# Kernel tuning notes

Hardware: AMD Instinct MI355X
Metric: run time of the kernel (lower is better)

## Reference

```python
import jax, jax.numpy as jnp
import numpy as np

# ----- module hyperparameters (from init_kwargs) -----
C = 21            # num_classes
H = 512           # image_dims[0]
W = 512           # image_dims[1]
THETA_ALPHA = 3.0 # bilateral spatial std
THETA_BETA = 3.0  # bilateral color std
THETA_GAMMA = 3.0 # spatial-only std
NUM_ITERS = 5
R_BIL = int(2 * THETA_ALPHA)   # bilateral window radius (2 sigma truncation)
R_SP = int(2 * THETA_GAMMA)    # spatial Gaussian radius


def _gauss_1d(radius, sigma):
    x = jnp.arange(-radius, radius + 1, dtype=jnp.float32)
    return jnp.exp(-0.5 * (x / sigma) ** 2)  # unnormalized; norm handled by norm_values


def spatial_filter(vals):
    """Separable truncated Gaussian blur over (H,W). vals: (C,H,W)."""
    k = _gauss_1d(R_SP, THETA_GAMMA)
    K = 2 * R_SP + 1
    x = vals[:, None]  # (C,1,H,W) -> treat channels as batch
    kh = k.reshape(1, 1, K, 1)
    kw = k.reshape(1, 1, 1, K)
    x = jax.lax.conv_general_dilated(x, kh, (1, 1), ((R_SP, R_SP), (0, 0)))
    x = jax.lax.conv_general_dilated(x, kw, (1, 1), ((0, 0), (R_SP, R_SP)))
    return x[:, 0]


def _bilateral_impl(vals, rgb):
    """Truncated-window bilateral Gaussian filter.
    vals: (C,H,W) values to filter; rgb: (3,H,W) guide image.
    weight(i,j) = exp(-0.5*(|p_i-p_j|^2/ta^2 + |I_i-I_j|^2/tb^2)) (symmetric kernel).
    """
    pad = R_BIL
    vp = jnp.pad(vals, ((0, 0), (pad, pad), (pad, pad)))
    rp = jnp.pad(rgb, ((0, 0), (pad, pad), (pad, pad)))
    d = jnp.arange(2 * pad + 1, dtype=jnp.int32)
    offs = jnp.stack(jnp.meshgrid(d, d, indexing='ij'), -1).reshape(-1, 2)  # (K^2,2)
    inv_a2 = 1.0 / (THETA_ALPHA ** 2)
    inv_b2 = 1.0 / (THETA_BETA ** 2)

    def step(acc, off):
        dy, dx = off[0], off[1]
        z = dy * 0
        srgb = jax.lax.dynamic_slice(rp, (z, dy, dx), rgb.shape)
        sval = jax.lax.dynamic_slice(vp, (z, dy, dx), vals.shape)
        dsp = ((dy - pad) ** 2 + (dx - pad) ** 2).astype(jnp.float32)
        dcol = jnp.sum((rgb - srgb) ** 2, axis=0)  # (H,W)
        w = jnp.exp(-0.5 * (dsp * inv_a2 + dcol * inv_b2))
        return acc + sval * w[None], None

    out, _ = jax.lax.scan(step, jnp.zeros_like(vals), offs)
    return out


# Symmetric linear operator in vals -> adjoint = same filter. rgb treated as constant
# (no grad to raw image, matching CRF-RNN training). Keeps backward memory O(1) in steps.
@jax.custom_vjp
def bilateral_filter(vals, rgb):
    return _bilateral_impl(vals, rgb)

def _bf_fwd(vals, rgb):
    return _bilateral_impl(vals, rgb), rgb

def _bf_bwd(rgb, g):
    return _bilateral_impl(g, rgb), jnp.zeros_like(rgb)

bilateral_filter.defvjp(_bf_fwd, _bf_bwd)


def setup_inputs() -> dict:
    key = jax.random.key(0)
    k1, k2, k3, k4 = jax.random.split(key, 4)
    unaries = jax.random.normal(k1, (1, H, W, C), jnp.float32)
    rgb = jax.random.uniform(k2, (1, H, W, 3), jnp.float32) * 255.0
    spatial_ker_weights = jax.random.uniform(k3, (C, C), jnp.float32)
    bilateral_ker_weights = jax.random.truncated_normal(k4, -2.0, 2.0, (C, C), jnp.float32)
    compatibility_matrix = -jnp.eye(C, dtype=jnp.float32)
    return {
        'unaries': unaries,
        'rgb': rgb,
        'spatial_ker_weights': spatial_ker_weights,
        'bilateral_ker_weights': bilateral_ker_weights,
        'compatibility_matrix': compatibility_matrix,
    }


def reference(unaries, rgb, spatial_ker_weights, bilateral_ker_weights, compatibility_matrix):
    u = jnp.transpose(unaries[0], (2, 1, 0))   # (C,W,H) as in tf.transpose perm=[2,1,0]
    im = jnp.transpose(rgb[0], (2, 1, 0))      # (3,W,H)
    c, h, w = u.shape
    ones = jnp.ones_like(u)
    sp_norm = spatial_filter(ones)
    bl_norm = bilateral_filter(ones, im)
    q = u
    for _ in range(NUM_ITERS):
        p = jax.nn.softmax(q, axis=0)
        sp = spatial_filter(p) / sp_norm
        bl = bilateral_filter(p, im) / bl_norm
        msg = spatial_ker_weights @ sp.reshape(c, -1) + bilateral_ker_weights @ bl.reshape(c, -1)
        pairwise = (compatibility_matrix @ msg).reshape(c, h, w)
        q = u - pairwise
    return jnp.transpose(q[None], (0, 2, 3, 1))  # (1,h,w,c)
```

## Files before the change

kernel.cpp:

```cpp
#include <hip/hip_runtime.h>
#include <cstddef>

#define HW   512
#define NPIX (HW*HW)
#define NP   (NPIX + 64)
#define NC   21

typedef unsigned int u32;
typedef __fp16 h2 __attribute__((ext_vector_type(2)));

__device__ __forceinline__ float fexp2(float x) { return __builtin_amdgcn_exp2f(x); }
__device__ __forceinline__ h2 as_h2(u32 x) { union { u32 u; h2 h; } v; v.u = x; return v.h; }
__device__ __forceinline__ u32 as_u32(h2 x) { union { h2 h; u32 u; } v; v.h = x; return v.u; }
__device__ __forceinline__ u32 pkrtz(float a, float b) { return as_u32(__builtin_amdgcn_cvt_pkrtz(a, b)); }

__device__ __forceinline__ float dot7(const u32* w, const u32* a, float s) {
    #pragma unroll
    for (int t = 0; t < 7; ++t)
        s = __builtin_amdgcn_fdot2(as_h2(w[t]), as_h2(a[t]), s, false);
    return s;
}

#define KB_EXP (-0.08014972449f)
#define LOG2E  (1.4426950408889634f)

#define KSP_INIT {0.13533528f, 0.24935221f, 0.41111229f, 0.60653066f, 0.80073740f, \
                  0.94595947f, 1.00000000f, 0.94595947f, 0.80073740f, 0.60653066f, \
                  0.41111229f, 0.24935221f, 0.13533528f}

__global__ void k_setup(const float* __restrict__ unaries, const float* __restrict__ rgb,
                        float* __restrict__ u, float* q, float* __restrict__ rgbT,
                        _Float16* u16) {
    int p = blockIdx.x * 256 + threadIdx.x;
    int a = p >> 9, b = p & 511;
    int src = b * 512 + a;
    #pragma unroll
    for (int c = 0; c < NC; ++c) {
        float v = unaries[src * NC + c];
        u[c * NP + p] = v;
        if (q)   q[c * NP + p] = v;
        if (u16) u16[(size_t)c * NPIX + p] = (_Float16)v;
    }
    #pragma unroll
    for (int ch = 0; ch < 3; ++ch) rgbT[ch * NP + p] = rgb[src * 3 + ch];
}

__global__ void k_prep(const float* __restrict__ Wsp, const float* __restrict__ Wbl,
                       const float* __restrict__ Cm,
                       float* __restrict__ invS, float* __restrict__ M1, float* __restrict__ M2) {
    int t = threadIdx.x;
    const float KSP[13] = KSP_INIT;
    {
        float s = 0.f;
        #pragma unroll
        for (int d = 0; d < 13; ++d) {
            int i = t + d - 6;
            if ((unsigned)i < 512u) s += KSP[d];
        }
        invS[t] = 1.0f / s;
    }
    if (t < NC * NC) {
        int c = t / NC, j = t % NC;
        float s1 = 0.f, s2 = 0.f;
        for (int k = 0; k < NC; ++k) {
            float cm = Cm[c * NC + k];
            s1 += cm * Wsp[k * NC + j];
            s2 += cm * Wbl[k * NC + j];
        }
        M1[t] = -s1;
        M2[t] = -s2;
    }
}

__global__ void k_weights(const float* __restrict__ rgbT, u32* __restrict__ wbuf,
                          float* __restrict__ inorm) {
    int a  = blockIdx.x;
    int b0 = threadIdx.x << 2;
    float cr[3][4];
    #pragma unroll
    for (int ch = 0; ch < 3; ++ch) {
        float4 f = *reinterpret_cast<const float4*>(rgbT + ch * NP + a * HW + b0);
        cr[ch][0] = f.x; cr[ch][1] = f.y; cr[ch][2] = f.z; cr[ch][3] = f.w;
    }
    float nsum[4] = {0.f, 0.f, 0.f, 0.f};
    #pragma unroll 1
    for (int dyi = 0; dyi < 13; ++dyi) {
        int ar = a + dyi - 6;
        if ((unsigned)ar >= 512u) continue;
        float nr[3][20];
        #pragma unroll
        for (int ch = 0; ch < 3; ++ch)
            #pragma unroll
            for (int tq = 0; tq < 5; ++tq) {
                float4 f = *reinterpret_cast<const float4*>(rgbT + ch * NP + ar * HW + b0 - 8 + 4 * tq);
                nr[ch][4*tq+0] = f.x; nr[ch][4*tq+1] = f.y; nr[ch][4*tq+2] = f.z; nr[ch][4*tq+3] = f.w;
            }
        float spk = KB_EXP * (float)((dyi - 6) * (dyi - 6));
        u32 arr[28];
        #pragma unroll
        for (int j = 0; j < 4; ++j) {
            float w[13];
            #pragma unroll
            for (int dx = 0; dx < 13; ++dx) {
                int ic = j + dx + 2;
                float d0 = cr[0][j] - nr[0][ic];
                float d1 = cr[1][j] - nr[1][ic];
                float d2 = cr[2][j] - nr[2][ic];
                float dcol = d0*d0 + d1*d1 + d2*d2;
                float arg = KB_EXP * dcol + (spk + KB_EXP * (float)((dx-6)*(dx-6)));
                bool ok = (unsigned)(b0 + j + dx - 6) < 512u;
                w[dx] = ok ? fexp2(arg) : 0.f;
                nsum[j] += w[dx];
            }
            #pragma unroll
            for (int t = 0; t < 6; ++t) arr[j*7+t] = pkrtz(w[2*t], w[2*t+1]);
            arr[j*7+6] = pkrtz(w[12], 0.f);
        }
        uint4* dst = reinterpret_cast<uint4*>(wbuf) + ((size_t)(a * 13 + dyi) * 896 + threadIdx.x * 7);
        #pragma unroll
        for (int k = 0; k < 7; ++k)
            dst[k] = make_uint4(arr[4*k], arr[4*k+1], arr[4*k+2], arr[4*k+3]);
    }
    float4 r;
    r.x = 1.0f / nsum[0]; r.y = 1.0f / nsum[1];
    r.z = 1.0f / nsum[2]; r.w = 1.0f / nsum[3];
    *reinterpret_cast<float4*>(inorm + a * HW + b0) = r;
}

__global__ __launch_bounds__(128, 3)
void k_filters(const _Float16* __restrict__ ph, const u32* __restrict__ wbuf,
               const float* __restrict__ invS,
               _Float16* __restrict__ P, _Float16* __restrict__ SP) {
    int bid = blockIdx.x;
    int xj = bid & 7;
    int g  = bid >> 3;
    int rl = g / 3;
    int y  = g - rl * 3;
    int a  = xj * 64 + rl;
    int cbase = y * 7;
    int tid = threadIdx.x;
    int b0  = tid << 2;

    const float KSP[13] = KSP_INIT;
    u32 kp[4][7];
    #pragma unroll
    for (int j = 0; j < 4; ++j) {
        float wj[13];
        #pragma unroll
        for (int dx = 0; dx < 13; ++dx) {
            bool ok = (unsigned)(b0 + j + dx - 6) < 512u;
            wj[dx] = ok ? KSP[dx] : 0.f;
        }
        #pragma unroll
        for (int t = 0; t < 6; ++t) kp[j][t] = pkrtz(wj[2*t], wj[2*t+1]);
        kp[j][6] = pkrtz(wj[12], 0.f);
    }

    float acc[7][4], spa[7][4];
    #pragma unroll
    for (int ci = 0; ci < 7; ++ci)
        #pragma unroll
        for (int j = 0; j < 4; ++j) { acc[ci][j] = 0.f; spa[ci][j] = 0.f; }

    #pragma unroll 1
    for (int dyi = 0; dyi < 13; ++dyi) {
        int ar = a + dyi - 6;
        if ((unsigned)ar >= 512u) continue;
        float kdy = fexp2(KB_EXP * (float)((dyi - 6) * (dyi - 6)));
        const uint4* wp = reinterpret_cast<const uint4*>(wbuf) + ((size_t)(a * 13 + dyi) * 896 + tid * 7);
        u32 arr[28];
        #pragma unroll
        for (int k = 0; k < 7; ++k) {
            uint4 wv = wp[k];
            arr[4*k] = wv.x; arr[4*k+1] = wv.y; arr[4*k+2] = wv.z; arr[4*k+3] = wv.w;
        }
        #pragma unroll
        for (int ci = 0; ci < 7; ++ci) {
            const uint2* pw = reinterpret_cast<const uint2*>(ph + (size_t)(cbase + ci) * NPIX + ar * HW + b0 - 8);
            uint2 L0 = pw[0], L1 = pw[1], L2 = pw[2], L3 = pw[3], L4 = pw[4];
            u32 W0[10] = {L0.x, L0.y, L1.x, L1.y, L2.x, L2.y, L3.x, L3.y, L4.x, L4.y};
            u32 W1[9];
            #pragma unroll
            for (int k = 1; k < 9; ++k) W1[k] = (W0[k] >> 16) | (W0[k+1] << 16);
            acc[ci][0] = dot7(arr + 0,  W0 + 1, acc[ci][0]);
            acc[ci][1] = dot7(arr + 7,  W1 + 1, acc[ci][1]);
            acc[ci][2] = dot7(arr + 14, W0 + 2, acc[ci][2]);
            acc[ci][3] = dot7(arr + 21, W1 + 2, acc[ci][3]);
            spa[ci][0] = fmaf(kdy, dot7(kp[0], W0 + 1, 0.f), spa[ci][0]);
            spa[ci][1] = fmaf(kdy, dot7(kp[1], W1 + 1, 0.f), spa[ci][1]);
            spa[ci][2] = fmaf(kdy, dot7(kp[2], W0 + 2, 0.f), spa[ci][2]);
            spa[ci][3] = fmaf(kdy, dot7(kp[3], W1 + 2, 0.f), spa[ci][3]);
        }
    }
    float isa = invS[a];
    float4 iv = *reinterpret_cast<const float4*>(invS + b0);
    #pragma unroll
    for (int ci = 0; ci < 7; ++ci) {
        uint2 st;
        st.x = pkrtz(acc[ci][0], acc[ci][1]);
        st.y = pkrtz(acc[ci][2], acc[ci][3]);
        *reinterpret_cast<uint2*>(P + (size_t)(cbase + ci) * NPIX + a * HW + b0) = st;
        uint2 ss;
        ss.x = pkrtz(spa[ci][0] * isa * iv.x, spa[ci][1] * isa * iv.y);
        ss.y = pkrtz(spa[ci][2] * isa * iv.z, spa[ci][3] * isa * iv.w);
        *reinterpret_cast<uint2*>(SP + (size_t)(cbase + ci) * NPIX + a * HW + b0) = ss;
    }
}

__global__ void k_combine2(const float* __restrict__ u, const _Float16* __restrict__ u16,
                           const _Float16* __restrict__ sp, const _Float16* __restrict__ P,
                           const float* __restrict__ inorm,
                           const float* __restrict__ M1, const float* __restrict__ M2,
                           _Float16* __restrict__ phout, float* __restrict__ out, int last) {
    __shared__ float m1[NC * NC], m2[NC * NC];
    int t = threadIdx.x;
    for (int i = t; i < NC * NC; i += 256) { m1[i] = M1[i]; m2[i] = M2[i]; }
    __syncthreads();
    int px = blockIdx.x * 256 + t;
    float rn = inorm[px];
    float msg[NC];
    #pragma unroll
    for (int c = 0; c < NC; ++c) msg[c] = 0.f;
    #pragma unroll 3
    for (int k = 0; k < NC; ++k) {
        float s = (float)sp[(size_t)k * NPIX + px];
        float b = (float)P[(size_t)k * NPIX + px] * rn;
        #pragma unroll
        for (int c = 0; c < NC; ++c) msg[c] += m1[c * NC + k] * s + m2[c * NC + k] * b;
    }
    if (last) {
        #pragma unroll
        for (int c = 0; c < NC; ++c)
            out[(size_t)px * NC + c] = u[c * NP + px] + msg[c];
    } else {
        float qv[NC];
        #pragma unroll
        for (int c = 0; c < NC; ++c) qv[c] = (float)u16[(size_t)c * NPIX + px] + msg[c];
        float m = -1e30f;
        #pragma unroll
        for (int c = 0; c < NC; ++c) m = fmaxf(m, qv[c]);
        float s = 0.f;
        #pragma unroll
        for (int c = 0; c < NC; ++c) { qv[c] = fexp2((qv[c] - m) * LOG2E); s += qv[c]; }
        float r = 1.0f / s;
        #pragma unroll
        for (int c = 0; c < NC; ++c) phout[(size_t)c * NPIX + px] = (_Float16)(qv[c] * r);
    }
}

__global__ void k_softmax(const float* __restrict__ q, _Float16* __restrict__ ph) {
    int i4 = (blockIdx.x * 256 + threadIdx.x) << 2;
    float v[NC][4];
    float m[4] = {-1e30f, -1e30f, -1e30f, -1e30f};
    #pragma unroll
    for (int c = 0; c < NC; ++c) {
        float4 f = *reinterpret_cast<const float4*>(q + c * NP + i4);
        v[c][0] = f.x; v[c][1] = f.y; v[c][2] = f.z; v[c][3] = f.w;
        #pragma unroll
        for (int j = 0; j < 4; ++j) m[j] = fmaxf(m[j], v[c][j]);
    }
    float s[4] = {0.f, 0.f, 0.f, 0.f};
    #pragma unroll
    for (int c = 0; c < NC; ++c)
        #pragma unroll
        for (int j = 0; j < 4; ++j) { v[c][j] = fexp2((v[c][j] - m[j]) * LOG2E); s[j] += v[c][j]; }
    float r[4];
    #pragma unroll
    for (int j = 0; j < 4; ++j) r[j] = 1.0f / s[j];
    #pragma unroll
    for (int c = 0; c < NC; ++c) {
        uint2 st;
        st.x = pkrtz(v[c][0] * r[0], v[c][1] * r[1]);
        st.y = pkrtz(v[c][2] * r[2], v[c][3] * r[3]);
        *reinterpret_cast<uint2*>(ph + (size_t)c * NPIX + i4) = st;
    }
}

__global__ void k_blnorm_part(const float* __restrict__ rgbT, float* __restrict__ nq) {
    int bid = blockIdx.x;
    int z = bid >> 9, a = bid & 511;
    int b0 = threadIdx.x << 2;
    float cr[3][4];
    #pragma unroll
    for (int ch = 0; ch < 3; ++ch) {
        float4 f = *reinterpret_cast<const float4*>(rgbT + ch * NP + a * HW + b0);
        cr[ch][0] = f.x; cr[ch][1] = f.y; cr[ch][2] = f.z; cr[ch][3] = f.w;
    }
    float sum[4] = {0.f, 0.f, 0.f, 0.f};
    const int dylos[4] = {-6, -3, 1, 4};
    const int dyhis[4] = {-4,  0, 3, 6};
    int dylo = dylos[z], dyhi = dyhis[z];
    #pragma unroll 1
    for (int dy = dylo; dy <= dyhi; ++dy) {
        int ar = a + dy;
        if ((unsigned)ar >= 512u) continue;
        int rowoff = ar * HW + b0 - 8;
        float nr[3][20];
        #pragma unroll
        for (int ch = 0; ch < 3; ++ch)
            #pragma unroll
            for (int tq = 0; tq < 5; ++tq) {
                float4 f = *reinterpret_cast<const float4*>(rgbT + ch * NP + rowoff + 4 * tq);
                nr[ch][4*tq+0] = f.x; nr[ch][4*tq+1] = f.y; nr[ch][4*tq+2] = f.z; nr[ch][4*tq+3] = f.w;
            }
        float spk = KB_EXP * (float)(dy * dy);
        #pragma unroll
        for (int j = 0; j < 4; ++j) {
            #pragma unroll
            for (int dx = 0; dx < 13; ++dx) {
                int ic = j + dx + 2;
                float d0 = cr[0][j] - nr[0][ic];
                float d1 = cr[1][j] - nr[1][ic];
                float d2 = cr[2][j] - nr[2][ic];
                float dcol = d0*d0 + d1*d1 + d2*d2;
                float arg = KB_EXP * dcol + (spk + KB_EXP * (float)((dx-6)*(dx-6)));
                bool ok = (unsigned)(b0 + j + dx - 6) < 512u;
                sum[j] += ok ? fexp2(arg) : 0.f;
            }
        }
    }
    float4 r; r.x = sum[0]; r.y = sum[1]; r.z = sum[2]; r.w = sum[3];
    *reinterpret_cast<float4*>(nq + (size_t)z * NP + a * HW + b0) = r;
}

__global__ void k_invnorm(const float* __restrict__ nq, float* __restrict__ inorm) {
    int i = blockIdx.x * 256 + threadIdx.x;
    inorm[i] = 1.0f / (nq[i] + nq[NP + i] + nq[2 * (size_t)NP + i] + nq[3 * (size_t)NP + i]);
}

__global__ void k_spatial_h(const _Float16* __restrict__ ph, _Float16* __restrict__ dst) {
    int idx = blockIdx.x * 256 + threadIdx.x;
    int b0 = (idx & 127) << 2;
    int a  = (idx >> 7) & 511;
    int c  = idx >> 16;
    const uint2* pw = reinterpret_cast<const uint2*>(ph + (size_t)c * NPIX + a * HW + b0 - 8);
    uint2 L0 = pw[0], L1 = pw[1], L2 = pw[2], L3 = pw[3], L4 = pw[4];
    u32 W0[10] = {L0.x, L0.y, L1.x, L1.y, L2.x, L2.y, L3.x, L3.y, L4.x, L4.y};
    const float KSP[13] = KSP_INIT;
    float out[4];
    if (b0 >= 8 && b0 <= 500) {
        u32 W1[9];
        #pragma unroll
        for (int k = 1; k < 9; ++k) W1[k] = (W0[k] >> 16) | (W0[k+1] << 16);
        u32 kp[7];
        #pragma unroll
        for (int t = 0; t < 6; ++t) kp[t] = pkrtz(KSP[2*t], KSP[2*t+1]);
        kp[6] = pkrtz(KSP[12], 0.f);
        out[0] = dot7(kp, W0 + 1, 0.f);
        out[1] = dot7(kp, W1 + 1, 0.f);
        out[2] = dot7(kp, W0 + 2, 0.f);
        out[3] = dot7(kp, W1 + 2, 0.f);
    } else {
        float pv[20];
        #pragma unroll
        for (int k = 0; k < 10; ++k) { h2 hh = as_h2(W0[k]); pv[2*k] = (float)hh[0]; pv[2*k+1] = (float)hh[1]; }
        #pragma unroll
        for (int j = 0; j < 4; ++j) out[j] = 0.f;
        #pragma unroll
        for (int d = 0; d < 13; ++d)
            #pragma unroll
            for (int j = 0; j < 4; ++j) {
                bool ok = (unsigned)(b0 + j + d - 6) < 512u;
                out[j] += (ok ? KSP[d] : 0.f) * pv[j + d + 2];
            }
    }
    uint2 st;
    st.x = pkrtz(out[0], out[1]);
    st.y = pkrtz(out[2], out[3]);
    *reinterpret_cast<uint2*>(dst + (size_t)c * NPIX + a * HW + b0) = st;
}

__global__ void k_spatial_v(const _Float16* __restrict__ src, _Float16* __restrict__ dst,
                            const float* __restrict__ invS) {
    int idx = blockIdx.x * 256 + threadIdx.x;
    int b0 = (idx & 127) << 2;
    int a  = (idx >> 7) & 511;
    int c  = idx >> 16;
    const float KSP[13] = KSP_INIT;
    float out[4] = {0.f, 0.f, 0.f, 0.f};
    #pragma unroll
    for (int d = 0; d < 13; ++d) {
        int ar = a + d - 6;
        if ((unsigned)ar < 512u) {
            uint2 L = *reinterpret_cast<const uint2*>(src + (size_t)c * NPIX + ar * HW + b0);
            h2 h0 = as_h2(L.x), h1 = as_h2(L.y);
            out[0] += KSP[d] * (float)h0[0]; out[1] += KSP[d] * (float)h0[1];
            out[2] += KSP[d] * (float)h1[0]; out[3] += KSP[d] * (float)h1[1];
        }
    }
    float isa = invS[a];
    float4 iv = *reinterpret_cast<const float4*>(invS + b0);
    uint2 st;
    st.x = pkrtz(out[0] * isa * iv.x, out[1] * isa * iv.y);
    st.y = pkrtz(out[2] * isa * iv.z, out[3] * isa * iv.w);
    *reinterpret_cast<uint2*>(dst + (size_t)c * NPIX + a * HW + b0) = st;
}

__global__ __launch_bounds__(128, 4)
void k_bilateral(const _Float16* __restrict__ ph, const float* __restrict__ rgbT,
                 float* __restrict__ P0, float* __restrict__ P1) {
    int bid = blockIdx.x;
    int xj = bid & 7;
    int g  = bid >> 3;
    int rl = g / 6;
    int v  = g - rl * 6;
    int a  = xj * 64 + rl;
    int y  = v >> 1;
    int z  = v & 1;
    int cbase = y * 7;
    int b0  = threadIdx.x << 2;
    float cr[3][4];
    #pragma unroll
    for (int ch = 0; ch < 3; ++ch) {
        float4 f = *reinterpret_cast<const float4*>(rgbT + ch * NP + a * HW + b0);
        cr[ch][0] = f.x; cr[ch][1] = f.y; cr[ch][2] = f.z; cr[ch][3] = f.w;
    }
    float acc[7][4];
    #pragma unroll
    for (int ci = 0; ci < 7; ++ci)
        #pragma unroll
        for (int j2 = 0; j2 < 4; ++j2) acc[ci][j2] = 0.f;

    int dylo = z ? 1 : -6, dyhi = z ? 6 : 0;
    #pragma unroll 1
    for (int dy = dylo; dy <= dyhi; ++dy) {
        int ar = a + dy;
        if ((unsigned)ar >= 512u) continue;
        float nr[3][20];
        #pragma unroll
        for (int ch = 0; ch < 3; ++ch)
            #pragma unroll
            for (int tq = 0; tq < 5; ++tq) {
                float4 f = *reinterpret_cast<const float4*>(rgbT + ch * NP + ar * HW + b0 - 8 + 4 * tq);
                nr[ch][4*tq+0] = f.x; nr[ch][4*tq+1] = f.y; nr[ch][4*tq+2] = f.z; nr[ch][4*tq+3] = f.w;
            }
        float spk = KB_EXP * (float)(dy * dy);
        u32 wpk[4][7];
        #pragma unroll
        for (int jj = 0; jj < 4; ++jj) {
            float w[13];
            #pragma unroll
            for (int dx = 0; dx < 13; ++dx) {
                int ic = jj + dx + 2;
                float d0 = cr[0][jj] - nr[0][ic];
                float d1 = cr[1][jj] - nr[1][ic];
                float d2 = cr[2][jj] - nr[2][ic];
                float dcol = d0*d0 + d1*d1 + d2*d2;
                float arg = KB_EXP * dcol + (spk + KB_EXP * (float)((dx-6)*(dx-6)));
                bool ok = (unsigned)(b0 + jj + dx - 6) < 512u;
                w[dx] = ok ? fexp2(arg) : 0.f;
            }
            #pragma unroll
            for (int t = 0; t < 6; ++t) wpk[jj][t] = pkrtz(w[2*t], w[2*t+1]);
            wpk[jj][6] = pkrtz(w[12], 0.f);
        }
        #pragma unroll
        for (int ci = 0; ci < 7; ++ci) {
            const uint2* pw = reinterpret_cast<const uint2*>(ph + (size_t)(cbase + ci) * NPIX + ar * HW + b0 - 8);
            uint2 L0 = pw[0], L1 = pw[1], L2 = pw[2], L3 = pw[3], L4 = pw[4];
            u32 W0[10] = {L0.x, L0.y, L1.x, L1.y, L2.x, L2.y, L3.x, L3.y, L4.x, L4.y};
            u32 W1[9];
            #pragma unroll
            for (int k = 1; k < 9; ++k) W1[k] = (W0[k] >> 16) | (W0[k+1] << 16);
            acc[ci][0] = dot7(wpk[0], W0 + 1, acc[ci][0]);
            acc[ci][1] = dot7(wpk[1], W1 + 1, acc[ci][1]);
            acc[ci][2] = dot7(wpk[2], W0 + 2, acc[ci][2]);
            acc[ci][3] = dot7(wpk[3], W1 + 2, acc[ci][3]);
        }
    }
    float* dst = z ? P1 : P0;
    #pragma unroll
    for (int ci = 0; ci < 7; ++ci) {
        float4 r;
        r.x = acc[ci][0]; r.y = acc[ci][1]; r.z = acc[ci][2]; r.w = acc[ci][3];
        *reinterpret_cast<float4*>(dst + (cbase + ci) * NP + a * HW + b0) = r;
    }
}

__global__ void k_combine(const float* __restrict__ u, const _Float16* __restrict__ sp,
                          const float* __restrict__ P0, const float* __restrict__ P1,
                          const float* __restrict__ inorm,
                          const float* __restrict__ M1, const float* __restrict__ M2,
                          float* __restrict__ q) {
    __shared__ float m1[NC * NC], m2[NC * NC];
    int t = threadIdx.x;
    for (int i = t; i < NC * NC; i += 256) { m1[i] = M1[i]; m2[i] = M2[i]; }
    __syncthreads();
    int px = blockIdx.x * 256 + t;
    float rn = inorm[px];
    float msg[NC];
    #pragma unroll
    for (int c = 0; c < NC; ++c) msg[c] = 0.f;
    #pragma unroll 3
    for (int k = 0; k < NC; ++k) {
        float s = (float)sp[(size_t)k * NPIX + px];
        float b = (P0[k * NP + px] + P1[k * NP + px]) * rn;
        #pragma unroll
        for (int c = 0; c < NC; ++c) msg[c] += m1[c * NC + k] * s + m2[c * NC + k] * b;
    }
    #pragma unroll
    for (int c = 0; c < NC; ++c) q[c * NP + px] = u[c * NP + px] + msg[c];
}

__global__ void k_output(const float* __restrict__ q, float* __restrict__ out) {
    __shared__ float tile[256 * NC];
    int t = threadIdx.x;
    int p0 = blockIdx.x * 256;
    #pragma unroll
    for (int c = 0; c < NC; ++c) tile[t * NC + c] = q[c * NP + p0 + t];
    __syncthreads();
    for (int i = t; i < 256 * NC; i += 256) out[(size_t)p0 * NC + i] = tile[i];
}

extern "C" void kernel_launch(void* const* d_in, const int* in_sizes, int n_in,
                              void* d_out, int out_size, void* d_ws, size_t ws_size,
                              hipStream_t stream) {
    const float* unaries = (const float*)d_in[0];
    const float* rgb     = (const float*)d_in[1];
    const float* Wsp     = (const float*)d_in[2];
    const float* Wbl     = (const float*)d_in[3];
    const float* Cm      = (const float*)d_in[4];
    float* out = (float*)d_out;
    float* ws  = (float*)d_ws;

    const size_t PHF  = ((size_t)NC * NPIX + 128) / 2;
    const size_t WSZ  = (size_t)512 * 13 * 3584;
    const size_t BASE = (size_t)88 * NP + PHF + 2048;
    const size_t needed_fb   = BASE * sizeof(float);
    const size_t needed_fast = (BASE + WSZ) * sizeof(float);
    if (ws_size < needed_fb) return;
    bool fast = ws_size >= needed_fast;

    if (fast) {
        float* u     = ws;
        float* rgbT  = ws + (size_t)21 * NP;
        float* inorm = ws + (size_t)24 * NP;
        _Float16* u16  = (_Float16*)(ws + (size_t)25 * NP) + 64;
        _Float16* phsp = (_Float16*)(ws + (size_t)36 * NP) + 64;
        _Float16* sp16 = (_Float16*)(ws + (size_t)47 * NP) + 64;
        _Float16* P16  = (_Float16*)(ws + (size_t)58 * NP) + 64;
        float* invS  = ws + (size_t)69 * NP;
        float* M1    = invS + 512;
        float* M2    = M1 + 441;
        u32* wbuf    = (u32*)(ws + BASE);

        k_setup<<<NPIX / 256, 256, 0, stream>>>(unaries, rgb, u, nullptr, rgbT, u16);
        k_prep<<<1, 512, 0, stream>>>(Wsp, Wbl, Cm, invS, M1, M2);
        k_weights<<<512, 128, 0, stream>>>(rgbT, wbuf, inorm);
        k_softmax<<<NPIX / 4 / 256, 256, 0, stream>>>(u, phsp);

        for (int it = 0; it < 5; ++it) {
            k_filters<<<1536, 128, 0, stream>>>(phsp, wbuf, invS, P16, sp16);
            k_combine2<<<NPIX / 256, 256, 0, stream>>>(u, u16, sp16, P16, inorm,
                                                       M1, M2, phsp, out, it == 4);
        }
    } else {
        float* u     = ws;
        float* q     = ws + (size_t)21 * NP;
        float* A     = ws + (size_t)42 * NP;
        float* P1    = ws + (size_t)63 * NP;
        float* rgbT  = ws + (size_t)84 * NP;
        float* inorm = ws + (size_t)87 * NP;
        _Float16* ph = (_Float16*)(ws + (size_t)88 * NP) + 64;
        float* invS  = ws + (size_t)88 * NP + PHF;
        float* M1    = invS + 512;
        float* M2    = M1 + 441;
        _Float16* htmp = (_Float16*)q;
        _Float16* sp16 = ph;
        float* nq = P1;

        k_setup<<<NPIX / 256, 256, 0, stream>>>(unaries, rgb, u, q, rgbT, nullptr);
        k_prep<<<1, 512, 0, stream>>>(Wsp, Wbl, Cm, invS, M1, M2);
        k_blnorm_part<<<2048, 128, 0, stream>>>(rgbT, nq);
        k_invnorm<<<NPIX / 256, 256, 0, stream>>>(nq, inorm);

        for (int it = 0; it < 5; ++it) {
            k_softmax<<<NPIX / 4 / 256, 256, 0, stream>>>(q, ph);
            k_spatial_h<<<(NC * 512 * 128) / 256, 256, 0, stream>>>(ph, htmp);
            k_bilateral<<<3072, 128, 0, stream>>>(ph, rgbT, A, P1);
            k_spatial_v<<<(NC * 512 * 128) / 256, 256, 0, stream>>>(htmp, sp16, invS);
            k_combine<<<NPIX / 256, 256, 0, stream>>>(u, sp16, A, P1, inorm, M1, M2, q);
        }
        k_output<<<NPIX / 256, 256, 0, stream>>>(q, out);
    }
}
```

Measured before the change: 497.4 us.

## Fuse bilateral/spatial filtering with message combine and softmax per row

Merges the filter kernel and the combine/softmax kernel into one kernel where each 256-thread block handles a full image row for all 21 classes (2 pixels per thread). The fp16 filtered intermediates P and SP no longer round-trip through global memory, and a ping-pong buffer pair replaces the in-place probability update. The weight buffer layout is rearranged to match two pixels per thread. The trade-off is only 512 blocks, with 84 float accumulators plus 42 msg values per thread, so register pressure and occupancy may drop.

```diff
diff --git a/kernel.cpp b/kernel.cpp
--- a/kernel.cpp
+++ b/kernel.cpp
@@ -116,10 +116,14 @@
             for (int t = 0; t < 6; ++t) arr[j*7+t] = pkrtz(w[2*t], w[2*t+1]);
             arr[j*7+6] = pkrtz(w[12], 0.f);
         }
-        uint4* dst = reinterpret_cast<uint4*>(wbuf) + ((size_t)(a * 13 + dyi) * 896 + threadIdx.x * 7);
-        #pragma unroll
-        for (int k = 0; k < 7; ++k)
-            dst[k] = make_uint4(arr[4*k], arr[4*k+1], arr[4*k+2], arr[4*k+3]);
+        u32* slot = wbuf + (size_t)(a * 13 + dyi) * 3584;
+        #pragma unroll
+        for (int h = 0; h < 2; ++h) {
+            uint2* d = reinterpret_cast<uint2*>(slot) + ((threadIdx.x << 1) + h) * 7;
+            #pragma unroll
+            for (int k = 0; k < 7; ++k)
+                d[k] = make_uint2(arr[14*h + 2*k], arr[14*h + 2*k + 1]);
+        }
     }
     float4 r;
     r.x = 1.0f / nsum[0]; r.y = 1.0f / nsum[1];
@@ -127,124 +131,116 @@
     *reinterpret_cast<float4*>(inorm + a * HW + b0) = r;
 }
 
-__global__ __launch_bounds__(128, 3)
-void k_filters(const _Float16* __restrict__ ph, const u32* __restrict__ wbuf,
-               const float* __restrict__ invS,
-               _Float16* __restrict__ P, _Float16* __restrict__ SP) {
+__global__ __launch_bounds__(256)
+void k_fused(const _Float16* __restrict__ ph, const u32* __restrict__ wbuf,
+             const float* __restrict__ invS, const float* __restrict__ inorm,
+             const float* __restrict__ u, const _Float16* __restrict__ u16,
+             const float* __restrict__ M1, const float* __restrict__ M2,
+             _Float16* __restrict__ phout, float* __restrict__ out, int last) {
+    __shared__ float m1[NC * NC], m2[NC * NC];
+    int t = threadIdx.x;
+    for (int i = t; i < NC * NC; i += 256) { m1[i] = M1[i]; m2[i] = M2[i]; }
+    __syncthreads();
+
     int bid = blockIdx.x;
-    int xj = bid & 7;
-    int g  = bid >> 3;
-    int rl = g / 3;
-    int y  = g - rl * 3;
-    int a  = xj * 64 + rl;
-    int cbase = y * 7;
-    int tid = threadIdx.x;
-    int b0  = tid << 2;
+    int a = (bid & 7) * 64 + (bid >> 3);
+    int b0 = t << 1;
 
     const float KSP[13] = KSP_INIT;
-    u32 kp[4][7];
-    #pragma unroll
-    for (int j = 0; j < 4; ++j) {
-        float wj[13];
+    u32 kp0[7], kp1[7];
+    {
+        float w0[13], w1[13];
         #pragma unroll
         for (int dx = 0; dx < 13; ++dx) {
-            bool ok = (unsigned)(b0 + j + dx - 6) < 512u;
-            wj[dx] = ok ? KSP[dx] : 0.f;
-        }
-        #pragma unroll
-        for (int t = 0; t < 6; ++t) kp[j][t] = pkrtz(wj[2*t], wj[2*t+1]);
-        kp[j][6] = pkrtz(wj[12], 0.f);
-    }
-
-    float acc[7][4], spa[7][4];
-    #pragma unroll
-    for (int ci = 0; ci < 7; ++ci)
-        #pragma unroll
-        for (int j = 0; j < 4; ++j) { acc[ci][j] = 0.f; spa[ci][j] = 0.f; }
+            w0[dx] = ((unsigned)(b0 + dx - 6) < 512u)     ? KSP[dx] : 0.f;
+            w1[dx] = ((unsigned)(b0 + 1 + dx - 6) < 512u) ? KSP[dx] : 0.f;
+        }
+        #pragma unroll
+        for (int k = 0; k < 6; ++k) {
+            kp0[k] = pkrtz(w0[2*k], w0[2*k+1]);
+            kp1[k] = pkrtz(w1[2*k], w1[2*k+1]);
+        }
+        kp0[6] = pkrtz(w0[12], 0.f);
+        kp1[6] = pkrtz(w1[12], 0.f);
+    }
+
+    float acc[NC][2], spa[NC][2];
+    #pragma unroll
+    for (int c = 0; c < NC; ++c) { acc[c][0]=0.f; acc[c][1]=0.f; spa[c][0]=0.f; spa[c][1]=0.f; }
 
     #pragma unroll 1
     for (int dyi = 0; dyi < 13; ++dyi) {
         int ar = a + dyi - 6;
         if ((unsigned)ar >= 512u) continue;
         float kdy = fexp2(KB_EXP * (float)((dyi - 6) * (dyi - 6)));
-        const uint4* wp = reinterpret_cast<const uint4*>(wbuf) + ((size_t)(a * 13 + dyi) * 896 + tid * 7);
-        u32 arr[28];
-        #pragma unroll
-        for (int k = 0; k < 7; ++k) {
-            uint4 wv = wp[k];
-            arr[4*k] = wv.x; arr[4*k+1] = wv.y; arr[4*k+2] = wv.z; arr[4*k+3] = wv.w;
-        }
-        #pragma unroll
-        for (int ci = 0; ci < 7; ++ci) {
-            const uint2* pw = reinterpret_cast<const uint2*>(ph + (size_t)(cbase + ci) * NPIX + ar * HW + b0 - 8);
+        const uint2* wp = reinterpret_cast<const uint2*>(wbuf + (size_t)(a * 13 + dyi) * 3584) + t * 7;
+        u32 arr[14];
+        #pragma unroll
+        for (int k = 0; k < 7; ++k) { uint2 v = wp[k]; arr[2*k] = v.x; arr[2*k+1] = v.y; }
+        #pragma unroll
+        for (int ci = 0; ci < NC; ++ci) {
+            const uint2* pw = reinterpret_cast<const uint2*>(ph + (size_t)ci * NPIX + ar * HW + b0 - 8);
             uint2 L0 = pw[0], L1 = pw[1], L2 = pw[2], L3 = pw[3], L4 = pw[4];
             u32 W0[10] = {L0.x, L0.y, L1.x, L1.y, L2.x, L2.y, L3.x, L3.y, L4.x, L4.y};
-            u32 W1[9];
-            #pragma unroll
-            for (int k = 1; k < 9; ++k) W1[k] = (W0[k] >> 16) | (W0[k+1] << 16);
-            acc[ci][0] = dot7(arr + 0,  W0 + 1, acc[ci][0]);
-            acc[ci][1] = dot7(arr + 7,  W1 + 1, acc[ci][1]);
-            acc[ci][2] = dot7(arr + 14, W0 + 2, acc[ci][2]);
-            acc[ci][3] = dot7(arr + 21, W1 + 2, acc[ci][3]);
-            spa[ci][0] = fmaf(kdy, dot7(kp[0], W0 + 1, 0.f), spa[ci][0]);
-            spa[ci][1] = fmaf(kdy, dot7(kp[1], W1 + 1, 0.f), spa[ci][1]);
-            spa[ci][2] = fmaf(kdy, dot7(kp[2], W0 + 2, 0.f), spa[ci][2]);
-            spa[ci][3] = fmaf(kdy, dot7(kp[3], W1 + 2, 0.f), spa[ci][3]);
-        }
-    }
+            u32 W1[8];
+            #pragma unroll
+            for (int k = 1; k < 8; ++k) W1[k] = (W0[k] >> 16) | (W0[k+1] << 16);
+            acc[ci][0] = dot7(arr,     W0 + 1, acc[ci][0]);
+            acc[ci][1] = dot7(arr + 7, W1 + 1, acc[ci][1]);
+            spa[ci][0] = fmaf(kdy, dot7(kp0, W0 + 1, 0.f), spa[ci][0]);
+            spa[ci][1] = fmaf(kdy, dot7(kp1, W1 + 1, 0.f), spa[ci][1]);
+        }
+    }
+
+    int px = a * HW + b0;
+    float2 rn = *reinterpret_cast<const float2*>(inorm + px);
     float isa = invS[a];
-    float4 iv = *reinterpret_cast<const float4*>(invS + b0);
-    #pragma unroll
-    for (int ci = 0; ci < 7; ++ci) {
-        uint2 st;
-        st.x = pkrtz(acc[ci][0], acc[ci][1]);
-        st.y = pkrtz(acc[ci][2], acc[ci][3]);
-        *reinterpret_cast<uint2*>(P + (size_t)(cbase + ci) * NPIX + a * HW + b0) = st;
-        uint2 ss;
-        ss.x = pkrtz(spa[ci][0] * isa * iv.x, spa[ci][1] * isa * iv.y);
-        ss.y = pkrtz(spa[ci][2] * isa * iv.z, spa[ci][3] * isa * iv.w);
-        *reinterpret_cast<uint2*>(SP + (size_t)(cbase + ci) * NPIX + a * HW + b0) = ss;
-    }
-}
-
-__global__ void k_combine2(const float* __restrict__ u, const _Float16* __restrict__ u16,
-                           const _Float16* __restrict__ sp, const _Float16* __restrict__ P,
-                           const float* __restrict__ inorm,
-                           const float* __restrict__ M1, const float* __restrict__ M2,
-                           _Float16* __restrict__ phout, float* __restrict__ out, int last) {
-    __shared__ float m1[NC * NC], m2[NC * NC];
-    int t = threadIdx.x;
-    for (int i = t; i < NC * NC; i += 256) { m1[i] = M1[i]; m2[i] = M2[i]; }
-    __syncthreads();
-    int px = blockIdx.x * 256 + t;
-    float rn = inorm[px];
-    float msg[NC];
-    #pragma unroll
-    for (int c = 0; c < NC; ++c) msg[c] = 0.f;
+    float iv0 = invS[b0] * isa, iv1 = invS[b0 + 1] * isa;
+
+    float msg[NC][2];
+    #pragma unroll
+    for (int c = 0; c < NC; ++c) { msg[c][0] = 0.f; msg[c][1] = 0.f; }
     #pragma unroll 3
     for (int k = 0; k < NC; ++k) {
-        float s = (float)sp[(size_t)k * NPIX + px];
-        float b = (float)P[(size_t)k * NPIX + px] * rn;
-        #pragma unroll
-        for (int c = 0; c < NC; ++c) msg[c] += m1[c * NC + k] * s + m2[c * NC + k] * b;
-    }
+        float s0 = spa[k][0] * iv0, s1 = spa[k][1] * iv1;
+        float bl0 = acc[k][0] * rn.x, bl1 = acc[k][1] * rn.y;
+        #pragma unroll
+        for (int c = 0; c < NC; ++c) {
+            float a1 = m1[c * NC + k], a2 = m2[c * NC + k];
+            msg[c][0] += a1 * s0 + a2 * bl0;
+            msg[c][1] += a1 * s1 + a2 * bl1;
+        }
+    }
+
     if (last) {
         #pragma unroll
+        for (int c = 0; c < NC; ++c) {
+            float2 uu = *reinterpret_cast<const float2*>(u + c * NP + px);
+            out[(size_t)px * NC + c]       = uu.x + msg[c][0];
+            out[(size_t)(px + 1) * NC + c] = uu.y + msg[c][1];
+        }
+    } else {
+        float q0[NC], q1[NC];
+        #pragma unroll
+        for (int c = 0; c < NC; ++c) {
+            u32 uv = *reinterpret_cast<const u32*>(u16 + (size_t)c * NPIX + px);
+            h2 uh = as_h2(uv);
+            q0[c] = (float)uh[0] + msg[c][0];
+            q1[c] = (float)uh[1] + msg[c][1];
+        }
+        float m0 = -1e30f, m1v = -1e30f;
+        #pragma unroll
+        for (int c = 0; c < NC; ++c) { m0 = fmaxf(m0, q0[c]); m1v = fmaxf(m1v, q1[c]); }
+        float s0 = 0.f, s1 = 0.f;
+        #pragma unroll
+        for (int c = 0; c < NC; ++c) {
+            q0[c] = fexp2((q0[c] - m0) * LOG2E);  s0 += q0[c];
+            q1[c] = fexp2((q1[c] - m1v) * LOG2E); s1 += q1[c];
+        }
+        float r0 = 1.0f / s0, r1 = 1.0f / s1;
+        #pragma unroll
         for (int c = 0; c < NC; ++c)
-            out[(size_t)px * NC + c] = u[c * NP + px] + msg[c];
-    } else {
-        float qv[NC];
-        #pragma unroll
-        for (int c = 0; c < NC; ++c) qv[c] = (float)u16[(size_t)c * NPIX + px] + msg[c];
-        float m = -1e30f;
-        #pragma unroll
-        for (int c = 0; c < NC; ++c) m = fmaxf(m, qv[c]);
-        float s = 0.f;
-        #pragma unroll
-        for (int c = 0; c < NC; ++c) { qv[c] = fexp2((qv[c] - m) * LOG2E); s += qv[c]; }
-        float r = 1.0f / s;
-        #pragma unroll
-        for (int c = 0; c < NC; ++c) phout[(size_t)c * NPIX + px] = (_Float16)(qv[c] * r);
+            *reinterpret_cast<u32*>(phout + (size_t)c * NPIX + px) = pkrtz(q0[c] * r0, q1[c] * r1);
     }
 }
 
@@ -535,10 +531,9 @@
         float* u     = ws;
         float* rgbT  = ws + (size_t)21 * NP;
         float* inorm = ws + (size_t)24 * NP;
-        _Float16* u16  = (_Float16*)(ws + (size_t)25 * NP) + 64;
-        _Float16* phsp = (_Float16*)(ws + (size_t)36 * NP) + 64;
-        _Float16* sp16 = (_Float16*)(ws + (size_t)47 * NP) + 64;
-        _Float16* P16  = (_Float16*)(ws + (size_t)58 * NP) + 64;
+        _Float16* u16 = (_Float16*)(ws + (size_t)25 * NP) + 64;
+        _Float16* phA = (_Float16*)(ws + (size_t)36 * NP) + 64;
+        _Float16* phB = (_Float16*)(ws + (size_t)47 * NP) + 64;
         float* invS  = ws + (size_t)69 * NP;
         float* M1    = invS + 512;
         float* M2    = M1 + 441;
@@ -547,12 +542,14 @@
         k_setup<<<NPIX / 256, 256, 0, stream>>>(unaries, rgb, u, nullptr, rgbT, u16);
         k_prep<<<1, 512, 0, stream>>>(Wsp, Wbl, Cm, invS, M1, M2);
         k_weights<<<512, 128, 0, stream>>>(rgbT, wbuf, inorm);
-        k_softmax<<<NPIX / 4 / 256, 256, 0, stream>>>(u, phsp);
-
+        k_softmax<<<NPIX / 4 / 256, 256, 0, stream>>>(u, phA);
+
+        _Float16* cur = phA;
+        _Float16* nxt = phB;
         for (int it = 0; it < 5; ++it) {
-            k_filters<<<1536, 128, 0, stream>>>(phsp, wbuf, invS, P16, sp16);
-            k_combine2<<<NPIX / 256, 256, 0, stream>>>(u, u16, sp16, P16, inorm,
-                                                       M1, M2, phsp, out, it == 4);
+            k_fused<<<512, 256, 0, stream>>>(cur, wbuf, invS, inorm, u, u16,
+                                             M1, M2, nxt, out, it == 4);
+            _Float16* tmp = cur; cur = nxt; nxt = tmp;
         }
     } else {
         float* u     = ws;
```

Result: slower. 771.5 us (+55.1%).
